# Performance work log

Measured on AMD Instinct MI355X. Metric: run time of the kernel, lower is better.

Reference implementation:

```python
import jax, jax.numpy as jnp
import numpy as np

D_MODEL = 1024
D_FF = 4096
N_HEADS = 16
EPS = 1e-5


def setup_inputs() -> dict:
    key = jax.random.key(0)
    ks = jax.random.split(key, 12)
    s = 0.02
    inp = {
        "x": jax.random.normal(ks[0], (4, 2048, D_MODEL), dtype=jnp.float32),
        "Wq": jax.random.normal(ks[1], (D_MODEL, D_MODEL), dtype=jnp.float32) * s,
        "bq": jnp.zeros((D_MODEL,), jnp.float32),
        "Wk": jax.random.normal(ks[2], (D_MODEL, D_MODEL), dtype=jnp.float32) * s,
        "bk": jnp.zeros((D_MODEL,), jnp.float32),
        "Wv": jax.random.normal(ks[3], (D_MODEL, D_MODEL), dtype=jnp.float32) * s,
        "bv": jnp.zeros((D_MODEL,), jnp.float32),
        "Wo": jax.random.normal(ks[4], (D_MODEL, D_MODEL), dtype=jnp.float32) * s,
        "bo": jnp.zeros((D_MODEL,), jnp.float32),
        "ln1_g": jnp.ones((D_MODEL,), jnp.float32),
        "ln1_b": jnp.zeros((D_MODEL,), jnp.float32),
        "ln2_g": jnp.ones((D_MODEL,), jnp.float32),
        "ln2_b": jnp.zeros((D_MODEL,), jnp.float32),
        "W1": jax.random.normal(ks[5], (D_MODEL, D_FF), dtype=jnp.float32) * s,
        "b1": jnp.zeros((D_FF,), jnp.float32),
        "W2": jax.random.normal(ks[6], (D_FF, D_MODEL), dtype=jnp.float32) * s,
        "b2": jnp.zeros((D_MODEL,), jnp.float32),
    }
    return inp


def _layernorm(x, g, b):
    mu = jnp.mean(x, axis=-1, keepdims=True)
    var = jnp.mean(jnp.square(x - mu), axis=-1, keepdims=True)
    return (x - mu) * jax.lax.rsqrt(var + EPS) * g + b


def _block(x, Wq, bq, Wk, bk, Wv, bv, Wo, bo, ln1_g, ln1_b, ln2_g, ln2_b, W1, b1, W2, b2):
    B, S, D = x.shape
    H = N_HEADS
    dk = D // H
    # --- sub_layer1: LN -> MHA ---
    h = _layernorm(x, ln1_g, ln1_b)
    q = (h @ Wq + bq).reshape(B, S, H, dk).transpose(0, 2, 1, 3)  # [B,H,S,dk]
    k = (h @ Wk + bk).reshape(B, S, H, dk).transpose(0, 2, 1, 3)
    v = (h @ Wv + bv).reshape(B, S, H, dk).transpose(0, 2, 1, 3)
    scores = jnp.einsum('bhqd,bhkd->bhqk', q, k) / jnp.sqrt(jnp.float32(dk))
    attn = jax.nn.softmax(scores, axis=-1)
    o = jnp.einsum('bhqk,bhkd->bhqd', attn, v)  # [B,H,S,dk]
    o = o.transpose(0, 2, 1, 3).reshape(B, S, D)
    x = x + (o @ Wo + bo)
    # --- sub_layer2: LN -> MLP (exact GELU) ---
    h = _layernorm(x, ln2_g, ln2_b)
    h = jax.nn.gelu(h @ W1 + b1, approximate=False)
    x = x + (h @ W2 + b2)
    return x


def reference(x, Wq, bq, Wk, bk, Wv, bv, Wo, bo, ln1_g, ln1_b, ln2_g, ln2_b, W1, b1, W2, b2):
    return _block(x, Wq, bq, Wk, bk, Wv, bv, Wo, bo, ln1_g, ln1_b, ln2_g, ln2_b, W1, b1, W2, b2)
```

## Files before the change

kernel.cpp:

```cpp
#include <hip/hip_runtime.h>
#include <hip/hip_bf16.h>
#include <math.h>

#define DM   1024
#define DFF  4096
#define NHEAD 16
#define DKH  64
#define SEQ  2048
#define NBATCH 4
#define NTOK 8192

typedef __attribute__((ext_vector_type(8))) __bf16 bf16x8;
typedef __attribute__((ext_vector_type(8))) short short8;
typedef __attribute__((ext_vector_type(4))) float f32x4;
typedef __attribute__((ext_vector_type(16))) float f32x16;
typedef __attribute__((ext_vector_type(4))) unsigned int u32x4;
typedef __attribute__((ext_vector_type(4))) unsigned short ushort4v;

__device__ __forceinline__ unsigned short f2bf(float f) {
    unsigned u = __builtin_bit_cast(unsigned, f);
    u += 0x7fffu + ((u >> 16) & 1u);
    return (unsigned short)(u >> 16);
}

__device__ __forceinline__ void gload_lds16(const void* g, void* l) {
    __builtin_amdgcn_global_load_lds(
        (const __attribute__((address_space(1))) unsigned int*)g,
        (__attribute__((address_space(3))) unsigned int*)l, 16, 0, 0);
}

__global__ __launch_bounds__(256) void transpose_cvt(
        const float* __restrict__ src, unsigned short* __restrict__ dst, int R, int C) {
    __shared__ unsigned short tile[32][33];
    const int c0 = blockIdx.x * 32, r0 = blockIdx.y * 32;
    const int tx = threadIdx.x & 31, ty = threadIdx.x >> 5;
    #pragma unroll
    for (int j = 0; j < 32; j += 8)
        tile[ty + j][tx] = f2bf(src[(size_t)(r0 + ty + j) * C + (c0 + tx)]);
    __syncthreads();
    #pragma unroll
    for (int j = 0; j < 32; j += 8)
        dst[(size_t)(c0 + ty + j) * R + (r0 + tx)] = tile[tx][ty + j];
}

__global__ __launch_bounds__(256) void concat_bias(
        const float* __restrict__ a, const float* __restrict__ b,
        const float* __restrict__ c, float* __restrict__ out) {
    int i = blockIdx.x * 256 + threadIdx.x;
    out[i] = (i < 1024) ? a[i] : (i < 2048 ? b[i - 1024] : c[i - 2048]);
}

__global__ __launch_bounds__(256) void ln_kernel(
        const float* __restrict__ x, const float* __restrict__ g,
        const float* __restrict__ b, unsigned short* __restrict__ out) {
    const int row = blockIdx.x, t = threadIdx.x;
    const float4 v = ((const float4*)(x + (size_t)row * DM))[t];
    float s1 = v.x + v.y + v.z + v.w;
    float s2 = v.x * v.x + v.y * v.y + v.z * v.z + v.w * v.w;
    #pragma unroll
    for (int off = 32; off > 0; off >>= 1) {
        s1 += __shfl_xor(s1, off, 64);
        s2 += __shfl_xor(s2, off, 64);
    }
    __shared__ float w1[4], w2[4];
    const int wid = t >> 6, lane = t & 63;
    if (lane == 0) { w1[wid] = s1; w2[wid] = s2; }
    __syncthreads();
    s1 = w1[0] + w1[1] + w1[2] + w1[3];
    s2 = w2[0] + w2[1] + w2[2] + w2[3];
    const float mu = s1 * (1.0f / DM);
    const float rs = rsqrtf(s2 * (1.0f / DM) - mu * mu + 1e-5f);
    const float4 gv = ((const float4*)g)[t];
    const float4 bv = ((const float4*)b)[t];
    ushort4v o;
    o[0] = f2bf((v.x - mu) * rs * gv.x + bv.x);
    o[1] = f2bf((v.y - mu) * rs * gv.y + bv.y);
    o[2] = f2bf((v.z - mu) * rs * gv.z + bv.z);
    o[3] = f2bf((v.w - mu) * rs * gv.w + bv.w);
    *(ushort4v*)(out + (size_t)row * DM + t * 4) = o;
}

#define LGKM0 do { asm volatile("s_waitcnt lgkmcnt(0)" ::: "memory"); \
                   __builtin_amdgcn_sched_barrier(0); } while (0)
#define SB0   __builtin_amdgcn_sched_barrier(0)

template<int BM, int BN, int EP>
__global__ __launch_bounds__(512, 2) void gemm8p(
        const unsigned short* __restrict__ A, const unsigned short* __restrict__ BT,
        const float* __restrict__ bias, const float* __restrict__ res,
        void* __restrict__ outp, int M, int N, int K) {
    constexpr int WM = BM / 2, WN = BN / 4;
    constexpr int MR = WM / 16, NR = WN / 16;
    constexpr int MH = MR / 2;
    constexpr int LA = BM / 64, LB = BN / 64;

    const int t = threadIdx.x;
    const int lane = t & 63, wid = t >> 6;
    const int wr = wid >> 2, wc = wid & 3;
    const int m0 = blockIdx.y * BM, n0 = blockIdx.x * BN;
    const int NT = K >> 6;

    __shared__ alignas(16) short As[2 * BM * 64];
    __shared__ alignas(16) short Bs[2 * BN * 64];

    const int srow = t >> 3, schk = t & 7;
    const int sw = ((schk ^ (srow & 7)) << 3);
    const unsigned short* gA = A  + (size_t)(m0 + srow) * K + (schk << 3);
    const unsigned short* gB = BT + (size_t)(n0 + srow) * K + (schk << 3);

    bf16x8 rA[LA], rB[LB];
    bf16x8 fa[MH][2], fb[4][2];
    f32x4 acc[MR][NR] = {};

    auto LOADA = [&](int tile) {
        const unsigned short* p = gA + tile * 64;
        #pragma unroll
        for (int j = 0; j < LA; ++j) rA[j] = *(const bf16x8*)(p + (size_t)j * 64 * K);
    };
    auto LOADB = [&](int tile) {
        const unsigned short* p = gB + tile * 64;
        #pragma unroll
        for (int j = 0; j < LB; ++j) rB[j] = *(const bf16x8*)(p + (size_t)j * 64 * K);
    };
    auto WRA = [&](int q) {
        short* d = As + q * (BM * 64) + srow * 64 + sw;
        #pragma unroll
        for (int j = 0; j < LA; ++j) *(bf16x8*)(d + j * 4096) = rA[j];
    };
    auto WRB = [&](int q) {
        short* d = Bs + q * (BN * 64) + srow * 64 + sw;
        #pragma unroll
        for (int j = 0; j < LB; ++j) *(bf16x8*)(d + j * 4096) = rB[j];
    };
    auto RDA = [&](int p, int mh) {
        const short* base = As + p * (BM * 64);
        #pragma unroll
        for (int m = 0; m < MH; ++m) {
            const int row = wr * WM + (mh * MH + m) * 16 + (lane & 15);
            #pragma unroll
            for (int kk = 0; kk < 2; ++kk)
                fa[m][kk] = *(const bf16x8*)(base + row * 64 +
                    ((((kk << 2) | (lane >> 4)) ^ (lane & 7)) << 3));
        }
    };
    auto RDB = [&](int p, int nh) {
        const short* base = Bs + p * (BN * 64);
        #pragma unroll
        for (int n = 0; n < 2; ++n) {
            const int row = wc * WN + (nh * 2 + n) * 16 + (lane & 15);
            #pragma unroll
            for (int kk = 0; kk < 2; ++kk)
                fb[nh * 2 + n][kk] = *(const bf16x8*)(base + row * 64 +
                    ((((kk << 2) | (lane >> 4)) ^ (lane & 7)) << 3));
        }
    };

#define MMA(mh, nh)                                                            \
    do {                                                                       \
        _Pragma("unroll")                                                      \
        for (int m_ = 0; m_ < MH; ++m_)                                        \
            _Pragma("unroll")                                                  \
            for (int n_ = 0; n_ < 2; ++n_)                                     \
                _Pragma("unroll")                                              \
                for (int kk_ = 0; kk_ < 2; ++kk_)                              \
                    acc[(mh) * MH + m_][(nh) * 2 + n_] =                       \
                        __builtin_amdgcn_mfma_f32_16x16x32_bf16(               \
                            fa[m_][kk_], fb[(nh) * 2 + n_][kk_],               \
                            acc[(mh) * MH + m_][(nh) * 2 + n_], 0, 0, 0);      \
    } while (0)

    LOADA(0); SB0; LOADB(0);
    asm volatile("s_waitcnt vmcnt(0)" ::: "memory");
    WRA(0); WRB(0);
    LOADA(NT > 1 ? 1 : 0); SB0; LOADB(NT > 1 ? 1 : 0);
    asm volatile("s_waitcnt lgkmcnt(0)" ::: "memory");
    SB0;
    __builtin_amdgcn_s_barrier();
    asm volatile("" ::: "memory");

    for (int tt = 0; tt < NT; ++tt) {
        const int p = tt & 1, q = p ^ 1;
        const int tp2 = (tt + 2 < NT) ? tt + 2 : NT - 1;
        RDA(p, 0); RDB(p, 0);
        LGKM0;
        __builtin_amdgcn_s_setprio(1); MMA(0, 0); __builtin_amdgcn_s_setprio(0);
        RDB(p, 1);
        asm volatile("s_waitcnt vmcnt(4)" ::: "memory");
        WRA(q);
        LGKM0;
        LOADA(tp2);
        SB0;
        __builtin_amdgcn_s_setprio(1); MMA(0, 1); __builtin_amdgcn_s_setprio(0);
        RDA(p, 1);
        if constexpr (LA == 4) { asm volatile("s_waitcnt vmcnt(4)" ::: "memory"); }
        else                   { asm volatile("s_waitcnt vmcnt(2)" ::: "memory"); }
        WRB(q);
        LGKM0;
        LOADB(tp2);
        SB0;
        __builtin_amdgcn_s_setprio(1); MMA(1, 1); __builtin_amdgcn_s_setprio(0);
        __builtin_amdgcn_s_setprio(1); MMA(1, 0); __builtin_amdgcn_s_setprio(0);
        __builtin_amdgcn_s_barrier();
        asm volatile("" ::: "memory");
    }
#undef MMA

    const int r_base = m0 + wr * WM + ((lane >> 4) << 2);
    const int c_base = n0 + wc * WN + (lane & 15);

    if constexpr (EP == 4) {
        unsigned short* qP = (unsigned short*)outp;
        unsigned short* kP = qP + (size_t)NTOK * 1024;
        unsigned short* vP = qP + (size_t)2 * NTOK * 1024;
        const int b  = m0 >> 11;
        const int sb = (m0 & 2047) + wr * WM + ((lane >> 4) << 2);
        #pragma unroll
        for (int ni = 0; ni < NR; ++ni) {
            const int col = c_base + ni * 16;
            const int which = col >> 10;
            const int h = (col >> 6) & 15;
            const int d = col & 63;
            const float bv = bias[col];
            const size_t bh = (size_t)(b * NHEAD + h);
            if (which < 2) {
                unsigned short* dst = (which ? kP : qP) + bh * SEQ * 64 + d;
                #pragma unroll
                for (int mi = 0; mi < MR; ++mi)
                    #pragma unroll
                    for (int i = 0; i < 4; ++i)
                        dst[(size_t)(sb + mi * 16 + i) * 64] = f2bf(acc[mi][ni][i] + bv);
            } else {
                unsigned short* dst = vP + bh * SEQ * 64;
                #pragma unroll
                for (int mi = 0; mi < MR; ++mi) {
                    const int s0 = sb + mi * 16;
                    ushort4v o;
                    #pragma unroll
                    for (int i = 0; i < 4; ++i) o[i] = f2bf(acc[mi][ni][i] + bv);
                    *(ushort4v*)(dst + (s0 >> 5) * 2048 + d * 32 + (s0 & 31)) = o;
                }
            }
        }
        return;
    }

    #pragma unroll
    for (int ni = 0; ni < NR; ++ni) {
        const int col = c_base + ni * 16;
        const float bv = bias[col];
        #pragma unroll
        for (int mi = 0; mi < MR; ++mi) {
            #pragma unroll
            for (int i = 0; i < 4; ++i) {
                const int row = r_base + mi * 16 + i;
                const size_t idx = (size_t)row * N + col;
                float v = acc[mi][ni][i] + bv;
                if (EP == 1 || EP == 3) v += res[idx];
                if (EP == 2) v = 0.5f * v * (1.0f + erff(v * 0.70710678118f));
                if (EP == 0 || EP == 2) ((unsigned short*)outp)[idx] = f2bf(v);
                else                    ((float*)outp)[idx] = v;
            }
        }
    }
}

__global__ __launch_bounds__(256, 4) void attn_kernel(
        const unsigned short* __restrict__ qP, const unsigned short* __restrict__ kP,
        const unsigned short* __restrict__ vP, unsigned short* __restrict__ o) {
    const int lane = threadIdx.x & 63;
    const int wid  = threadIdx.x >> 6;
    const int l31  = lane & 31;
    const int hi   = lane >> 5;
    const int bh = blockIdx.y;
    const int b = bh >> 4, h = bh & 15;
    const int q0 = blockIdx.x * 128 + wid * 32;

    __shared__ short Ks[2][2048];
    __shared__ short Vs[2][2048];
    __shared__ float lsum[4][32];

    bf16x8 qf[4];
    {
        const unsigned short* qp = qP + ((size_t)bh * SEQ + q0 + l31) * 64 + hi * 8;
        #pragma unroll
        for (int s = 0; s < 4; ++s) qf[s] = *(const bf16x8*)(qp + 16 * s);
    }

    const int krow  = wid * 8 + (lane >> 3);
    const int k_src = krow * 64 + (((lane & 7) ^ (lane >> 3)) << 3);
    const int vrow  = wid * 16 + (lane >> 2);
    const int v_src = vrow * 32 + (((lane & 3) ^ ((vrow >> 1) & 3)) << 3);
    const unsigned short* kb = kP + (size_t)bh * SEQ * 64 + k_src;
    const unsigned short* vb = vP + (size_t)bh * SEQ * 64 + v_src;
    short* ksd = &Ks[0][0] + wid * 512;
    short* vsd = &Vs[0][0] + wid * 512;

    auto STAGE = [&](int buf, int kv0) {
        gload_lds16(kb + (size_t)kv0 * 64, ksd + buf * 2048);
        gload_lds16(vb + (size_t)(kv0 >> 5) * 2048, vsd + buf * 2048);
    };

    STAGE(0, 0);
    asm volatile("s_waitcnt vmcnt(0)" ::: "memory");
    __builtin_amdgcn_s_barrier();

    f32x16 oacc0 = {}, oacc1 = {};
    float m_r = -1e30f, l_r = 0.0f;
    const float CE = 0.18033688011f;

    for (int kv0 = 0; kv0 < SEQ; kv0 += 32) {
        const int cur = (kv0 >> 5) & 1;
        if (kv0 + 32 < SEQ) STAGE(cur ^ 1, kv0 + 32);

        const short* kc = &Ks[cur][0];
        const short* vc = &Vs[cur][0];
        bf16x8 kf[4], vf[2][2];
        #pragma unroll
        for (int s = 0; s < 4; ++s)
            kf[s] = *(const bf16x8*)(kc + l31 * 64 + (((2 * s + hi) ^ (l31 & 7)) << 3));
        #pragma unroll
        for (int s = 0; s < 2; ++s)
            #pragma unroll
            for (int n = 0; n < 2; ++n) {
                const int d = l31 + 32 * n;
                vf[s][n] = *(const bf16x8*)(vc + d * 32 + (((2 * s + hi) ^ ((d >> 1) & 3)) << 3));
            }

        f32x16 S = {};
        #pragma unroll
        for (int s = 0; s < 4; ++s)
            S = __builtin_amdgcn_mfma_f32_32x32x16_bf16(kf[s], qf[s], S, 0, 0, 0);

        float t8[8];
        #pragma unroll
        for (int j = 0; j < 8; ++j) t8[j] = fmaxf(S[j], S[j + 8]);
        float tm = fmaxf(fmaxf(fmaxf(t8[0], t8[4]), fmaxf(t8[1], t8[5])),
                         fmaxf(fmaxf(t8[2], t8[6]), fmaxf(t8[3], t8[7])));
        tm = fmaxf(tm, __shfl_xor(tm, 32, 64));
        if (!__all(tm - m_r <= 44.0f)) {
            const float mn = fmaxf(m_r, tm);
            const float es = exp2f((m_r - mn) * CE);
            l_r *= es;
            #pragma unroll
            for (int r = 0; r < 16; ++r) { oacc0[r] *= es; oacc1[r] *= es; }
            m_r = mn;
        }
        float p[16];
        #pragma unroll
        for (int r = 0; r < 16; ++r) p[r] = exp2f((S[r] - m_r) * CE);
        float a8[8];
        #pragma unroll
        for (int j = 0; j < 8; ++j) a8[j] = p[j] + p[j + 8];
        float rs = ((a8[0] + a8[4]) + (a8[1] + a8[5])) + ((a8[2] + a8[6]) + (a8[3] + a8[7]));
        rs += __shfl_xor(rs, 32, 64);
        l_r += rs;

        unsigned pk[8];
        #pragma unroll
        for (int i = 0; i < 8; ++i) {
            unsigned rr;
            asm("v_cvt_pk_bf16_f32 %0, %1, %2" : "=v"(rr) : "v"(p[2 * i]), "v"(p[2 * i + 1]));
            pk[i] = rr;
        }
        asm volatile("v_permlane32_swap_b32 %0, %1" : "+v"(pk[0]), "+v"(pk[2]));
        asm volatile("v_permlane32_swap_b32 %0, %1" : "+v"(pk[1]), "+v"(pk[3]));
        asm volatile("v_permlane32_swap_b32 %0, %1" : "+v"(pk[4]), "+v"(pk[6]));
        asm volatile("v_permlane32_swap_b32 %0, %1" : "+v"(pk[5]), "+v"(pk[7]));
        const bf16x8 A0 = __builtin_bit_cast(bf16x8, (u32x4){pk[0], pk[1], pk[2], pk[3]});
        const bf16x8 A1 = __builtin_bit_cast(bf16x8, (u32x4){pk[4], pk[5], pk[6], pk[7]});

        oacc0 = __builtin_amdgcn_mfma_f32_32x32x16_bf16(A0, vf[0][0], oacc0, 0, 0, 0);
        oacc1 = __builtin_amdgcn_mfma_f32_32x32x16_bf16(A0, vf[0][1], oacc1, 0, 0, 0);
        oacc0 = __builtin_amdgcn_mfma_f32_32x32x16_bf16(A1, vf[1][0], oacc0, 0, 0, 0);
        oacc1 = __builtin_amdgcn_mfma_f32_32x32x16_bf16(A1, vf[1][1], oacc1, 0, 0, 0);

        asm volatile("s_waitcnt vmcnt(0)" ::: "memory");
        __builtin_amdgcn_s_barrier();
    }

    if (lane < 32) lsum[wid][l31] = 1.0f / l_r;
    float inv[16];
    #pragma unroll
    for (int r = 0; r < 16; ++r)
        inv[r] = lsum[wid][(r & 3) + 8 * (r >> 2) + 4 * hi];

    unsigned short* op = o + (size_t)(b * SEQ + q0) * DM + h * 64 + l31;
    #pragma unroll
    for (int r = 0; r < 16; ++r) {
        const int q = (r & 3) + 8 * (r >> 2) + 4 * hi;
        op[(size_t)q * DM]      = f2bf(oacc0[r] * inv[r]);
        op[(size_t)q * DM + 32] = f2bf(oacc1[r] * inv[r]);
    }
}

extern "C" void kernel_launch(void* const* d_in, const int* in_sizes, int n_in,
                              void* d_out, int out_size, void* d_ws, size_t ws_size,
                              hipStream_t stream) {
    const float* x    = (const float*)d_in[0];
    const float* Wq   = (const float*)d_in[1];
    const float* bq   = (const float*)d_in[2];
    const float* Wk   = (const float*)d_in[3];
    const float* bk   = (const float*)d_in[4];
    const float* Wv   = (const float*)d_in[5];
    const float* bv   = (const float*)d_in[6];
    const float* Wo   = (const float*)d_in[7];
    const float* bo   = (const float*)d_in[8];
    const float* ln1g = (const float*)d_in[9];
    const float* ln1b = (const float*)d_in[10];
    const float* ln2g = (const float*)d_in[11];
    const float* ln2b = (const float*)d_in[12];
    const float* W1   = (const float*)d_in[13];
    const float* b1   = (const float*)d_in[14];
    const float* W2   = (const float*)d_in[15];
    const float* b2   = (const float*)d_in[16];

    char* ws = (char*)d_ws;
    size_t off = 0;
    auto alloc = [&](size_t bytes) {
        char* p = ws + off;
        off = (off + bytes + 255) & ~(size_t)255;
        return p;
    };
    unsigned short* wqkvT = (unsigned short*)alloc((size_t)3072 * 1024 * 2);
    unsigned short* woT   = (unsigned short*)alloc((size_t)1024 * 1024 * 2);
    unsigned short* w1T   = (unsigned short*)alloc((size_t)4096 * 1024 * 2);
    unsigned short* w2T   = (unsigned short*)alloc((size_t)1024 * 4096 * 2);
    float*          bqkv  = (float*)alloc((size_t)3072 * 4);
    unsigned short* hbuf  = (unsigned short*)alloc((size_t)NTOK * DM * 2);
    unsigned short* pack  = (unsigned short*)alloc((size_t)NTOK * 3072 * 2);
    unsigned short* obuf  = (unsigned short*)alloc((size_t)NTOK * DM * 2);
    float*          x2    = (float*)alloc((size_t)NTOK * DM * 4);
    unsigned short* h2    = (unsigned short*)alloc((size_t)NTOK * DM * 2);
    unsigned short* gbuf  = (unsigned short*)alloc((size_t)NTOK * DFF * 2);

    const unsigned short* qP = pack;
    const unsigned short* kP = pack + (size_t)NTOK * 1024;
    const unsigned short* vP = pack + (size_t)2 * NTOK * 1024;

    transpose_cvt<<<dim3(32, 32), 256, 0, stream>>>(Wq, wqkvT,                 1024, 1024);
    transpose_cvt<<<dim3(32, 32), 256, 0, stream>>>(Wk, wqkvT + 1024 * 1024,   1024, 1024);
    transpose_cvt<<<dim3(32, 32), 256, 0, stream>>>(Wv, wqkvT + 2 * 1024 * 1024, 1024, 1024);
    transpose_cvt<<<dim3(32, 32), 256, 0, stream>>>(Wo, woT,                   1024, 1024);
    transpose_cvt<<<dim3(128, 32), 256, 0, stream>>>(W1, w1T, 1024, 4096);
    transpose_cvt<<<dim3(32, 128), 256, 0, stream>>>(W2, w2T, 4096, 1024);
    concat_bias<<<12, 256, 0, stream>>>(bq, bk, bv, bqkv);

    ln_kernel<<<NTOK, 256, 0, stream>>>(x, ln1g, ln1b, hbuf);

    gemm8p<256, 256, 4><<<dim3(3072 / 256, NTOK / 256), 512, 0, stream>>>(
        hbuf, wqkvT, bqkv, nullptr, pack, NTOK, 3072, 1024);

    attn_kernel<<<dim3(SEQ / 128, NBATCH * NHEAD), 256, 0, stream>>>(qP, kP, vP, obuf);

    gemm8p<128, 256, 1><<<dim3(1024 / 256, NTOK / 128), 512, 0, stream>>>(
        obuf, woT, bo, x, x2, NTOK, 1024, 1024);

    ln_kernel<<<NTOK, 256, 0, stream>>>(x2, ln2g, ln2b, h2);

    gemm8p<256, 256, 2><<<dim3(4096 / 256, NTOK / 256), 512, 0, stream>>>(
        h2, w1T, b1, nullptr, gbuf, NTOK, 4096, 1024);

    gemm8p<128, 256, 3><<<dim3(1024 / 256, NTOK / 128), 512, 0, stream>>>(
        gbuf, w2T, b2, x2, d_out, NTOK, 1024, 4096);

    (void)in_sizes; (void)n_in; (void)out_size; (void)ws_size;
}
```

Before: 613.5 us.

## Stage GEMM tiles via direct global-to-LDS loads with barrier-split MFMA phases

Replaces the register-staged global-load-then-LDS-write pipeline in the bf16 GEMM with direct global_load_lds 16-byte transfers, issuing next-tile chunks interleaved between MFMA quarters and gated by vmcnt and workgroup barriers. This removes VGPR staging and explicit LDS writes, aiming to cut register pressure and overlap memory with compute more evenly. It adds many more s_barrier calls per K-step, which may introduce synchronisation stalls. The QKV projection also switches from 256x256 to 128x256 tiles, doubling the grid.

```diff
diff --git a/kernel.cpp b/kernel.cpp
--- a/kernel.cpp
+++ b/kernel.cpp
@@ -28,6 +28,10 @@
         (const __attribute__((address_space(1))) unsigned int*)g,
         (__attribute__((address_space(3))) unsigned int*)l, 16, 0, 0);
 }
+
+#define LGKM0 do { asm volatile("s_waitcnt lgkmcnt(0)" ::: "memory"); \
+                   __builtin_amdgcn_sched_barrier(0); } while (0)
+#define SB0   __builtin_amdgcn_sched_barrier(0)
 
 __global__ __launch_bounds__(256) void transpose_cvt(
         const float* __restrict__ src, unsigned short* __restrict__ dst, int R, int C) {
@@ -80,130 +84,125 @@
     *(ushort4v*)(out + (size_t)row * DM + t * 4) = o;
 }
 
-#define LGKM0 do { asm volatile("s_waitcnt lgkmcnt(0)" ::: "memory"); \
-                   __builtin_amdgcn_sched_barrier(0); } while (0)
-#define SB0   __builtin_amdgcn_sched_barrier(0)
-
 template<int BM, int BN, int EP>
-__global__ __launch_bounds__(512, 2) void gemm8p(
+__global__ __launch_bounds__(512, 2) void gemmp(
         const unsigned short* __restrict__ A, const unsigned short* __restrict__ BT,
         const float* __restrict__ bias, const float* __restrict__ res,
         void* __restrict__ outp, int M, int N, int K) {
     constexpr int WM = BM / 2, WN = BN / 4;
     constexpr int MR = WM / 16, NR = WN / 16;
-    constexpr int MH = MR / 2;
-    constexpr int LA = BM / 64, LB = BN / 64;
+    constexpr int MH = MR / 2, NH = NR / 2;
+    constexpr int CHA = BM / 64, CHB = BN / 64;
+    constexpr int VMN = CHA + CHB;
 
     const int t = threadIdx.x;
     const int lane = t & 63, wid = t >> 6;
     const int wr = wid >> 2, wc = wid & 3;
+    const int l15 = lane & 15, l7 = lane & 7, q4 = lane >> 4;
     const int m0 = blockIdx.y * BM, n0 = blockIdx.x * BN;
     const int NT = K >> 6;
 
     __shared__ alignas(16) short As[2 * BM * 64];
     __shared__ alignas(16) short Bs[2 * BN * 64];
 
-    const int srow = t >> 3, schk = t & 7;
-    const int sw = ((schk ^ (srow & 7)) << 3);
-    const unsigned short* gA = A  + (size_t)(m0 + srow) * K + (schk << 3);
-    const unsigned short* gB = BT + (size_t)(n0 + srow) * K + (schk << 3);
-
-    bf16x8 rA[LA], rB[LB];
-    bf16x8 fa[MH][2], fb[4][2];
+    const int srow = t >> 3;
+    const int swz8 = (((t & 7) ^ (srow & 7)) << 3);
+    const unsigned short* gAt = A  + (size_t)(m0 + srow) * K + swz8;
+    const unsigned short* gBt = BT + (size_t)(n0 + srow) * K + swz8;
+
+    bf16x8 fa[MH][2], fb[NR][2];
     f32x4 acc[MR][NR] = {};
 
-    auto LOADA = [&](int tile) {
-        const unsigned short* p = gA + tile * 64;
-        #pragma unroll
-        for (int j = 0; j < LA; ++j) rA[j] = *(const bf16x8*)(p + (size_t)j * 64 * K);
-    };
-    auto LOADB = [&](int tile) {
-        const unsigned short* p = gB + tile * 64;
-        #pragma unroll
-        for (int j = 0; j < LB; ++j) rB[j] = *(const bf16x8*)(p + (size_t)j * 64 * K);
-    };
-    auto WRA = [&](int q) {
-        short* d = As + q * (BM * 64) + srow * 64 + sw;
-        #pragma unroll
-        for (int j = 0; j < LA; ++j) *(bf16x8*)(d + j * 4096) = rA[j];
-    };
-    auto WRB = [&](int q) {
-        short* d = Bs + q * (BN * 64) + srow * 64 + sw;
-        #pragma unroll
-        for (int j = 0; j < LB; ++j) *(bf16x8*)(d + j * 4096) = rB[j];
-    };
-    auto RDA = [&](int p, int mh) {
-        const short* base = As + p * (BM * 64);
+    auto STG_A = [&](int tile, int ch) {
+        gload_lds16(gAt + (size_t)ch * 64 * K + (size_t)tile * 64,
+                    As + ((size_t)(tile & 1) * BM + ch * 64) * 64 + wid * 512);
+    };
+    auto STG_B = [&](int tile, int ch) {
+        gload_lds16(gBt + (size_t)ch * 64 * K + (size_t)tile * 64,
+                    Bs + ((size_t)(tile & 1) * BN + ch * 64) * 64 + wid * 512);
+    };
+    auto RD_FA = [&](int p, int mh) {
+        const short* base = As + (size_t)p * BM * 64;
         #pragma unroll
         for (int m = 0; m < MH; ++m) {
-            const int row = wr * WM + (mh * MH + m) * 16 + (lane & 15);
+            const int row = wr * WM + (mh * MH + m) * 16 + l15;
             #pragma unroll
             for (int kk = 0; kk < 2; ++kk)
-                fa[m][kk] = *(const bf16x8*)(base + row * 64 +
-                    ((((kk << 2) | (lane >> 4)) ^ (lane & 7)) << 3));
-        }
-    };
-    auto RDB = [&](int p, int nh) {
-        const short* base = Bs + p * (BN * 64);
-        #pragma unroll
-        for (int n = 0; n < 2; ++n) {
-            const int row = wc * WN + (nh * 2 + n) * 16 + (lane & 15);
+                fa[m][kk] = *(const bf16x8*)(base + row * 64 + (((kk * 4 + q4) ^ l7) << 3));
+        }
+    };
+    auto RD_FB = [&](int p, int nh) {
+        const short* base = Bs + (size_t)p * BN * 64;
+        #pragma unroll
+        for (int j = 0; j < NH; ++j) {
+            const int row = wc * WN + (nh * NH + j) * 16 + l15;
             #pragma unroll
             for (int kk = 0; kk < 2; ++kk)
-                fb[nh * 2 + n][kk] = *(const bf16x8*)(base + row * 64 +
-                    ((((kk << 2) | (lane >> 4)) ^ (lane & 7)) << 3));
-        }
-    };
-
-#define MMA(mh, nh)                                                            \
+                fb[nh * NH + j][kk] = *(const bf16x8*)(base + row * 64 + (((kk * 4 + q4) ^ l7) << 3));
+        }
+    };
+
+#define VMGATE do {                                                            \
+        if constexpr (VMN == 8) asm volatile("s_waitcnt vmcnt(8)" ::: "memory"); \
+        else                    asm volatile("s_waitcnt vmcnt(6)" ::: "memory"); \
+        __builtin_amdgcn_sched_barrier(0); } while (0)
+
+#define MMAQ(mh, nh)                                                           \
     do {                                                                       \
         _Pragma("unroll")                                                      \
         for (int m_ = 0; m_ < MH; ++m_)                                        \
             _Pragma("unroll")                                                  \
-            for (int n_ = 0; n_ < 2; ++n_)                                     \
+            for (int j_ = 0; j_ < NH; ++j_)                                    \
                 _Pragma("unroll")                                              \
                 for (int kk_ = 0; kk_ < 2; ++kk_)                              \
-                    acc[(mh) * MH + m_][(nh) * 2 + n_] =                       \
+                    acc[(mh) * MH + m_][(nh) * NH + j_] =                      \
                         __builtin_amdgcn_mfma_f32_16x16x32_bf16(               \
-                            fa[m_][kk_], fb[(nh) * 2 + n_][kk_],               \
-                            acc[(mh) * MH + m_][(nh) * 2 + n_], 0, 0, 0);      \
+                            fa[m_][kk_], fb[(nh) * NH + j_][kk_],              \
+                            acc[(mh) * MH + m_][(nh) * NH + j_], 0, 0, 0);     \
     } while (0)
 
-    LOADA(0); SB0; LOADB(0);
-    asm volatile("s_waitcnt vmcnt(0)" ::: "memory");
-    WRA(0); WRB(0);
-    LOADA(NT > 1 ? 1 : 0); SB0; LOADB(NT > 1 ? 1 : 0);
-    asm volatile("s_waitcnt lgkmcnt(0)" ::: "memory");
+    #pragma unroll
+    for (int ch = 0; ch < CHA; ++ch) STG_A(0, ch);
+    #pragma unroll
+    for (int ch = 0; ch < CHB; ++ch) STG_B(0, ch);
+    #pragma unroll
+    for (int ch = 0; ch < CHB; ++ch) STG_B(1, ch);
+    #pragma unroll
+    for (int ch = 0; ch < (CHA == 4 ? 2 : CHA); ++ch) STG_A(1, ch);
     SB0;
-    __builtin_amdgcn_s_barrier();
-    asm volatile("" ::: "memory");
-
-    for (int tt = 0; tt < NT; ++tt) {
-        const int p = tt & 1, q = p ^ 1;
-        const int tp2 = (tt + 2 < NT) ? tt + 2 : NT - 1;
-        RDA(p, 0); RDB(p, 0);
+
+    for (int T = 0; T < NT; ++T) {
+        const int p = T & 1;
+        if constexpr (CHA == 4) {
+            if (T + 1 < NT) { STG_A(T + 1, 2); STG_A(T + 1, 3); }
+        }
+        VMGATE;
+        RD_FA(p, 0); RD_FB(p, 0);
+        __builtin_amdgcn_s_barrier(); SB0;
         LGKM0;
-        __builtin_amdgcn_s_setprio(1); MMA(0, 0); __builtin_amdgcn_s_setprio(0);
-        RDB(p, 1);
-        asm volatile("s_waitcnt vmcnt(4)" ::: "memory");
-        WRA(q);
+        __builtin_amdgcn_s_setprio(1); MMAQ(0, 0); __builtin_amdgcn_s_setprio(0);
+        __builtin_amdgcn_s_barrier(); SB0;
+        RD_FB(p, 1);
+        __builtin_amdgcn_s_barrier(); SB0;
         LGKM0;
-        LOADA(tp2);
-        SB0;
-        __builtin_amdgcn_s_setprio(1); MMA(0, 1); __builtin_amdgcn_s_setprio(0);
-        RDA(p, 1);
-        if constexpr (LA == 4) { asm volatile("s_waitcnt vmcnt(4)" ::: "memory"); }
-        else                   { asm volatile("s_waitcnt vmcnt(2)" ::: "memory"); }
-        WRB(q);
+        __builtin_amdgcn_s_setprio(1); MMAQ(0, 1); __builtin_amdgcn_s_setprio(0);
+        __builtin_amdgcn_s_barrier(); SB0;
+        RD_FA(p, 1);
+        if (T + 2 < NT) { STG_B(T + 2, 0); STG_B(T + 2, 1); }
+        __builtin_amdgcn_s_barrier(); SB0;
         LGKM0;
-        LOADB(tp2);
-        SB0;
-        __builtin_amdgcn_s_setprio(1); MMA(1, 1); __builtin_amdgcn_s_setprio(0);
-        __builtin_amdgcn_s_setprio(1); MMA(1, 0); __builtin_amdgcn_s_setprio(0);
-        __builtin_amdgcn_s_barrier();
-        asm volatile("" ::: "memory");
-    }
-#undef MMA
+        __builtin_amdgcn_s_setprio(1); MMAQ(1, 1); __builtin_amdgcn_s_setprio(0);
+        __builtin_amdgcn_s_barrier(); SB0;
+        if (T + 2 < NT) {
+            STG_B(T + 2, 2); STG_B(T + 2, 3);
+            STG_A(T + 2, 0); STG_A(T + 2, 1);
+        }
+        __builtin_amdgcn_s_barrier(); SB0;
+        __builtin_amdgcn_s_setprio(1); MMAQ(1, 0); __builtin_amdgcn_s_setprio(0);
+        __builtin_amdgcn_s_barrier(); SB0;
+    }
+#undef MMAQ
+#undef VMGATE
 
     const int r_base = m0 + wr * WM + ((lane >> 4) << 2);
     const int c_base = n0 + wc * WN + (lane & 15);
@@ -447,20 +446,20 @@
 
     ln_kernel<<<NTOK, 256, 0, stream>>>(x, ln1g, ln1b, hbuf);
 
-    gemm8p<256, 256, 4><<<dim3(3072 / 256, NTOK / 256), 512, 0, stream>>>(
+    gemmp<128, 256, 4><<<dim3(3072 / 256, NTOK / 128), 512, 0, stream>>>(
         hbuf, wqkvT, bqkv, nullptr, pack, NTOK, 3072, 1024);
 
     attn_kernel<<<dim3(SEQ / 128, NBATCH * NHEAD), 256, 0, stream>>>(qP, kP, vP, obuf);
 
-    gemm8p<128, 256, 1><<<dim3(1024 / 256, NTOK / 128), 512, 0, stream>>>(
+    gemmp<128, 256, 1><<<dim3(1024 / 256, NTOK / 128), 512, 0, stream>>>(
         obuf, woT, bo, x, x2, NTOK, 1024, 1024);
 
     ln_kernel<<<NTOK, 256, 0, stream>>>(x2, ln2g, ln2b, h2);
 
-    gemm8p<256, 256, 2><<<dim3(4096 / 256, NTOK / 256), 512, 0, stream>>>(
+    gemmp<256, 256, 2><<<dim3(4096 / 256, NTOK / 256), 512, 0, stream>>>(
         h2, w1T, b1, nullptr, gbuf, NTOK, 4096, 1024);
 
-    gemm8p<128, 256, 3><<<dim3(1024 / 256, NTOK / 128), 512, 0, stream>>>(
+    gemmp<128, 256, 3><<<dim3(1024 / 256, NTOK / 128), 512, 0, stream>>>(
         gbuf, w2T, b2, x2, d_out, NTOK, 1024, 4096);
 
     (void)in_sizes; (void)n_in; (void)out_size; (void)ws_size;
```

Measured after the change: 619.2 us. No clear change (+0.9%).
